# Performance work log

Measured on AMD Instinct MI355X. Metric: run time of the kernel, lower is better.

The kernel has to match this reference:

```python
import jax, jax.numpy as jnp
import numpy as np

B, T, H, Z = 128, 1024, 256, 64


def setup_inputs() -> dict:
    key = jax.random.key(0)
    k1, k2, k3, k4 = jax.random.split(key, 4)
    scale = 1.0 / np.sqrt(H + Z)
    return {
        "input_q": jax.random.normal(k1, (B, T, H), dtype=jnp.float32),
        "eps": jax.random.normal(k2, (B, T, Z), dtype=jnp.float32),
        "W_mu": jax.random.normal(k3, (Z, H + Z), dtype=jnp.float32) * scale,
        "b_mu": jnp.zeros((Z,), dtype=jnp.float32),
        "W_std": jax.random.normal(k4, (Z, H + Z), dtype=jnp.float32) * scale,
        "b_std": jnp.zeros((Z,), dtype=jnp.float32),
    }


def reference(input_q, eps, W_mu, b_mu, W_std, b_std):
    # Recurrent sampling: z_t = mu(h_t, z_{t-1}) + eps_t * std(h_t, z_{t-1})
    h_seq = jnp.swapaxes(input_q, 0, 1)  # [T, B, H]
    e_seq = jnp.swapaxes(eps, 0, 1)      # [T, B, Z]

    def step(z_prev, inp):
        h_t, e_t = inp
        x = jnp.concatenate([h_t, z_prev], axis=-1)          # [B, H+Z]
        mu = x @ W_mu.T + b_mu                               # [B, Z]
        std = jax.nn.softplus(x @ W_std.T + b_std) + 1e-4    # [B, Z]
        z = mu + e_t * std
        return z, (z, mu, std)

    z0 = jnp.zeros((B, Z), dtype=input_q.dtype)
    _, (z_seq, mu_seq, std_seq) = jax.lax.scan(step, z0, (h_seq, e_seq))
    # stack outputs back to [B, T, Z]
    z_seq = jnp.swapaxes(z_seq, 0, 1)
    mu_seq = jnp.swapaxes(mu_seq, 0, 1)
    std_seq = jnp.swapaxes(std_seq, 0, 1)
    return (z_seq, mu_seq, std_seq)
```

## Files before the change

kernel.cpp:

```cpp
#include <hip/hip_runtime.h>
#include <math.h>

#define B_ 128
#define T_ 1024
#define H_ 256
#define Z_ 64
#define M_ (B_ * T_)

__global__ __launch_bounds__(256) void precompute_kernel(
    const float* __restrict__ Hm,
    const float* __restrict__ Wmu,
    const float* __restrict__ Wstd,
    const float* __restrict__ bmu,
    const float* __restrict__ bstd,
    float* __restrict__ pre_mu,
    float* __restrict__ pre_std)
{
    const int tid = threadIdx.x;
    const int ty = tid >> 4;
    const int tx = tid & 15;
    const int m0 = blockIdx.x * 64;

    __shared__ float Ash[64][17];
    __shared__ float Wm[64][17];
    __shared__ float Ws[64][17];

    float accm[4][4] = {};
    float accs[4][4] = {};

    const int lrow = tid >> 2;
    const int lk   = (tid & 3) * 4;

    for (int k0 = 0; k0 < 256; k0 += 16) {
        float4 av  = *reinterpret_cast<const float4*>(&Hm[(size_t)(m0 + lrow) * H_ + k0 + lk]);
        float4 wmv = *reinterpret_cast<const float4*>(&Wmu[(size_t)lrow * 320 + k0 + lk]);
        float4 wsv = *reinterpret_cast<const float4*>(&Wstd[(size_t)lrow * 320 + k0 + lk]);
        __syncthreads();
        Ash[lrow][lk + 0] = av.x;  Ash[lrow][lk + 1] = av.y;
        Ash[lrow][lk + 2] = av.z;  Ash[lrow][lk + 3] = av.w;
        Wm[lrow][lk + 0] = wmv.x;  Wm[lrow][lk + 1] = wmv.y;
        Wm[lrow][lk + 2] = wmv.z;  Wm[lrow][lk + 3] = wmv.w;
        Ws[lrow][lk + 0] = wsv.x;  Ws[lrow][lk + 1] = wsv.y;
        Ws[lrow][lk + 2] = wsv.z;  Ws[lrow][lk + 3] = wsv.w;
        __syncthreads();

        #pragma unroll
        for (int kk = 0; kk < 16; ++kk) {
            float a4[4], wm4[4], ws4[4];
            #pragma unroll
            for (int i = 0; i < 4; ++i) a4[i] = Ash[ty * 4 + i][kk];
            #pragma unroll
            for (int jj = 0; jj < 4; ++jj) wm4[jj] = Wm[tx * 4 + jj][kk];
            #pragma unroll
            for (int jj = 0; jj < 4; ++jj) ws4[jj] = Ws[tx * 4 + jj][kk];
            #pragma unroll
            for (int i = 0; i < 4; ++i)
                #pragma unroll
                for (int jj = 0; jj < 4; ++jj) {
                    accm[i][jj] += a4[i] * wm4[jj];
                    accs[i][jj] += a4[i] * ws4[jj];
                }
        }
    }

    float4 bm = *reinterpret_cast<const float4*>(&bmu[tx * 4]);
    float4 bs = *reinterpret_cast<const float4*>(&bstd[tx * 4]);
    #pragma unroll
    for (int i = 0; i < 4; ++i) {
        const size_t m = (size_t)(m0 + ty * 4 + i);
        float4 om, os;
        om.x = accm[i][0] + bm.x;  om.y = accm[i][1] + bm.y;
        om.z = accm[i][2] + bm.z;  om.w = accm[i][3] + bm.w;
        os.x = accs[i][0] + bs.x;  os.y = accs[i][1] + bs.y;
        os.z = accs[i][2] + bs.z;  os.w = accs[i][3] + bs.w;
        *reinterpret_cast<float4*>(&pre_mu[m * Z_ + tx * 4])  = om;
        *reinterpret_cast<float4*>(&pre_std[m * Z_ + tx * 4]) = os;
    }
}

__global__ __launch_bounds__(64)
__attribute__((amdgpu_waves_per_eu(1, 1)))
void recurrent_kernel(
    const float* __restrict__ pre_mu,
    const float* __restrict__ pre_std,
    const float* __restrict__ eps,
    const float* __restrict__ Wmu,
    const float* __restrict__ Wstd,
    float* __restrict__ out)
{
    const int b = blockIdx.x;
    const int j = threadIdx.x;

    float amu[64], astd[64];
    {
        const float4* wm4 = reinterpret_cast<const float4*>(&Wmu[(size_t)j * 320 + 256]);
        const float4* ws4 = reinterpret_cast<const float4*>(&Wstd[(size_t)j * 320 + 256]);
        #pragma unroll
        for (int k = 0; k < 16; ++k) {
            const float4 a = wm4[k];
            const float4 s = ws4[k];
            amu[4 * k + 0] = a.x;  amu[4 * k + 1] = a.y;
            amu[4 * k + 2] = a.z;  amu[4 * k + 3] = a.w;
            astd[4 * k + 0] = s.x; astd[4 * k + 1] = s.y;
            astd[4 * k + 2] = s.z; astd[4 * k + 3] = s.w;
        }
        #pragma unroll
        for (int k = 0; k < 64; ++k) {
            asm volatile("" : "+v"(amu[k]));
            asm volatile("" : "+v"(astd[k]));
        }
    }

    const size_t base = (size_t)b * T_ * Z_;
    float* __restrict__ zo   = out;
    float* __restrict__ muo  = out + (size_t)M_ * Z_;
    float* __restrict__ stdo = out + (size_t)2 * M_ * Z_;

    float pm = pre_mu[base + j];
    float ps = pre_std[base + j];
    float ev = eps[base + j];

    float z = 0.0f;

    for (int t = 0; t < T_; ++t) {
        float pm_n = 0.f, ps_n = 0.f, ev_n = 0.f;
        if (t + 1 < T_) {
            const size_t idx = base + (size_t)(t + 1) * Z_ + j;
            pm_n = pre_mu[idx];
            ps_n = pre_std[idx];
            ev_n = eps[idx];
        }

        const unsigned zb = __float_as_uint(z);
        float am0 = pm, am1 = 0.f, am2 = 0.f, am3 = 0.f;
        float as0 = ps, as1 = 0.f, as2 = 0.f, as3 = 0.f;
        #pragma unroll
        for (int k = 0; k < 16; ++k) {
            const float z0 = __uint_as_float(__builtin_amdgcn_readlane(zb, 4 * k + 0));
            const float z1 = __uint_as_float(__builtin_amdgcn_readlane(zb, 4 * k + 1));
            const float z2 = __uint_as_float(__builtin_amdgcn_readlane(zb, 4 * k + 2));
            const float z3 = __uint_as_float(__builtin_amdgcn_readlane(zb, 4 * k + 3));
            am0 += z0 * amu[4 * k + 0];  as0 += z0 * astd[4 * k + 0];
            am1 += z1 * amu[4 * k + 1];  as1 += z1 * astd[4 * k + 1];
            am2 += z2 * amu[4 * k + 2];  as2 += z2 * astd[4 * k + 2];
            am3 += z3 * amu[4 * k + 3];  as3 += z3 * astd[4 * k + 3];
        }
        const float mu = (am0 + am1) + (am2 + am3);
        const float sx = (as0 + as1) + (as2 + as3);
        const float sp = (sx > 20.0f) ? sx : __logf(1.0f + __expf(sx));
        const float sd = sp + 1e-4f;
        z = mu + ev * sd;

        const size_t o = base + (size_t)t * Z_ + j;
        zo[o]   = z;
        muo[o]  = mu;
        stdo[o] = sd;

        pm = pm_n; ps = ps_n; ev = ev_n;
    }
}

extern "C" void kernel_launch(void* const* d_in, const int* in_sizes, int n_in,
                              void* d_out, int out_size, void* d_ws, size_t ws_size,
                              hipStream_t stream) {
    const float* input_q = (const float*)d_in[0];
    const float* eps     = (const float*)d_in[1];
    const float* W_mu    = (const float*)d_in[2];
    const float* b_mu    = (const float*)d_in[3];
    const float* W_std   = (const float*)d_in[4];
    const float* b_std   = (const float*)d_in[5];
    float* out = (float*)d_out;

    float* pre_mu  = (float*)d_ws;
    float* pre_std = pre_mu + (size_t)M_ * Z_;

    precompute_kernel<<<M_ / 64, 256, 0, stream>>>(
        input_q, W_mu, W_std, b_mu, b_std, pre_mu, pre_std);

    recurrent_kernel<<<B_, 64, 0, stream>>>(
        pre_mu, pre_std, eps, W_mu, W_std, out);
}
```

Baseline: 648.6 us.

## Use LDS broadcast of z with packed FMA and two-step prefetch in recurrence

The recurrent kernel now writes z to a double-buffered shared array and reads it back as float2 pairs instead of issuing 64 readlane broadcasts per step. The dot products use v_pk_fma_f32 on packed weight registers, halving the FMA instruction count. Prefetch distance for pre_mu, pre_std and eps is raised to two steps to hide global load latency. In exchange it depends on LDS round-trip latency and an inline waitcnt with no barrier, which is safe only because the block is a single wavefront.

```diff
diff --git a/kernel.cpp b/kernel.cpp
--- a/kernel.cpp
+++ b/kernel.cpp
@@ -6,6 +6,8 @@
 #define H_ 256
 #define Z_ 64
 #define M_ (B_ * T_)
+
+typedef float v2f __attribute__((ext_vector_type(2)));
 
 __global__ __launch_bounds__(256) void precompute_kernel(
     const float* __restrict__ Hm,
@@ -91,7 +93,7 @@
     const int b = blockIdx.x;
     const int j = threadIdx.x;
 
-    float amu[64], astd[64];
+    v2f wmu2[32], wstd2[32];
     {
         const float4* wm4 = reinterpret_cast<const float4*>(&Wmu[(size_t)j * 320 + 256]);
         const float4* ws4 = reinterpret_cast<const float4*>(&Wstd[(size_t)j * 320 + 256]);
@@ -99,64 +101,74 @@
         for (int k = 0; k < 16; ++k) {
             const float4 a = wm4[k];
             const float4 s = ws4[k];
-            amu[4 * k + 0] = a.x;  amu[4 * k + 1] = a.y;
-            amu[4 * k + 2] = a.z;  amu[4 * k + 3] = a.w;
-            astd[4 * k + 0] = s.x; astd[4 * k + 1] = s.y;
-            astd[4 * k + 2] = s.z; astd[4 * k + 3] = s.w;
+            wmu2[2 * k + 0] = (v2f){a.x, a.y};
+            wmu2[2 * k + 1] = (v2f){a.z, a.w};
+            wstd2[2 * k + 0] = (v2f){s.x, s.y};
+            wstd2[2 * k + 1] = (v2f){s.z, s.w};
         }
         #pragma unroll
-        for (int k = 0; k < 64; ++k) {
-            asm volatile("" : "+v"(amu[k]));
-            asm volatile("" : "+v"(astd[k]));
+        for (int k = 0; k < 32; ++k) {
+            asm volatile("" : "+v"(wmu2[k]));
+            asm volatile("" : "+v"(wstd2[k]));
         }
     }
+
+    __shared__ __align__(16) float zs[2][64];
 
     const size_t base = (size_t)b * T_ * Z_;
     float* __restrict__ zo   = out;
     float* __restrict__ muo  = out + (size_t)M_ * Z_;
     float* __restrict__ stdo = out + (size_t)2 * M_ * Z_;
 
-    float pm = pre_mu[base + j];
-    float ps = pre_std[base + j];
-    float ev = eps[base + j];
+    float pm0 = pre_mu[base + j];
+    float ps0 = pre_std[base + j];
+    float ev0 = eps[base + j];
+    float pm1 = pre_mu[base + Z_ + j];
+    float ps1 = pre_std[base + Z_ + j];
+    float ev1 = eps[base + Z_ + j];
 
     float z = 0.0f;
 
     for (int t = 0; t < T_; ++t) {
-        float pm_n = 0.f, ps_n = 0.f, ev_n = 0.f;
-        if (t + 1 < T_) {
-            const size_t idx = base + (size_t)(t + 1) * Z_ + j;
-            pm_n = pre_mu[idx];
-            ps_n = pre_std[idx];
-            ev_n = eps[idx];
+        float* zrow = zs[t & 1];
+        zrow[j] = z;
+        asm volatile("s_waitcnt lgkmcnt(0)" ::: "memory");
+
+        float pm2 = 0.f, ps2 = 0.f, ev2 = 0.f;
+        if (t + 2 < T_) {
+            const size_t idx = base + (size_t)(t + 2) * Z_ + j;
+            pm2 = pre_mu[idx];
+            ps2 = pre_std[idx];
+            ev2 = eps[idx];
         }
 
-        const unsigned zb = __float_as_uint(z);
-        float am0 = pm, am1 = 0.f, am2 = 0.f, am3 = 0.f;
-        float as0 = ps, as1 = 0.f, as2 = 0.f, as3 = 0.f;
+        const v2f* __restrict__ z2 = reinterpret_cast<const v2f*>(zrow);
+        v2f am01 = (v2f){pm0, 0.f}, am23 = (v2f){0.f, 0.f};
+        v2f as01 = (v2f){ps0, 0.f}, as23 = (v2f){0.f, 0.f};
         #pragma unroll
         for (int k = 0; k < 16; ++k) {
-            const float z0 = __uint_as_float(__builtin_amdgcn_readlane(zb, 4 * k + 0));
-            const float z1 = __uint_as_float(__builtin_amdgcn_readlane(zb, 4 * k + 1));
-            const float z2 = __uint_as_float(__builtin_amdgcn_readlane(zb, 4 * k + 2));
-            const float z3 = __uint_as_float(__builtin_amdgcn_readlane(zb, 4 * k + 3));
-            am0 += z0 * amu[4 * k + 0];  as0 += z0 * astd[4 * k + 0];
-            am1 += z1 * amu[4 * k + 1];  as1 += z1 * astd[4 * k + 1];
-            am2 += z2 * amu[4 * k + 2];  as2 += z2 * astd[4 * k + 2];
-            am3 += z3 * amu[4 * k + 3];  as3 += z3 * astd[4 * k + 3];
+            const v2f za = z2[2 * k + 0];
+            const v2f zb = z2[2 * k + 1];
+            asm("v_pk_fma_f32 %0, %1, %2, %0" : "+v"(am01) : "v"(za), "v"(wmu2[2 * k + 0]));
+            asm("v_pk_fma_f32 %0, %1, %2, %0" : "+v"(as01) : "v"(za), "v"(wstd2[2 * k + 0]));
+            asm("v_pk_fma_f32 %0, %1, %2, %0" : "+v"(am23) : "v"(zb), "v"(wmu2[2 * k + 1]));
+            asm("v_pk_fma_f32 %0, %1, %2, %0" : "+v"(as23) : "v"(zb), "v"(wstd2[2 * k + 1]));
         }
-        const float mu = (am0 + am1) + (am2 + am3);
-        const float sx = (as0 + as1) + (as2 + as3);
+        const v2f amt = am01 + am23;
+        const v2f ast = as01 + as23;
+        const float mu = amt.x + amt.y;
+        const float sx = ast.x + ast.y;
         const float sp = (sx > 20.0f) ? sx : __logf(1.0f + __expf(sx));
         const float sd = sp + 1e-4f;
-        z = mu + ev * sd;
+        z = mu + ev0 * sd;
 
         const size_t o = base + (size_t)t * Z_ + j;
         zo[o]   = z;
         muo[o]  = mu;
         stdo[o] = sd;
 
-        pm = pm_n; ps = ps_n; ev = ev_n;
+        pm0 = pm1; ps0 = ps1; ev0 = ev1;
+        pm1 = pm2; ps1 = ps2; ev1 = ev2;
     }
 }
 
```

After: 646.9 us. Within noise of the previous version (-0.3%).
